# Performance work log

Hardware: AMD Instinct MI355X
Metric: run time of the kernel (lower is better)

## Reference

```python
import jax, jax.numpy as jnp
import numpy as np
import math

B, W, V, D, H, L = 64, 255, 16389, 512, 8, 8
S = W + 1          # window + cls token
NLOC = V - 5       # n_locations
CLS = V - 1        # cls_index = 16388
DH = D // H
FF = 4 * D


def _pe(seq_len, d):
    # Faithful to the quirky PositionalEmbedding: for even col c, sin(pos/10000**(2c/d));
    # for odd col c (= i+1), cos(pos/10000**(2c/d)) since it uses 2*(i+1)/d.
    pos = np.arange(seq_len, dtype=np.float32)[:, None]
    c = np.arange(d, dtype=np.float32)[None, :]
    ang = pos / (10000.0 ** (2.0 * c / d))
    pe = np.where(np.arange(d)[None, :] % 2 == 0, np.sin(ang), np.cos(ang))
    return jnp.asarray(pe, jnp.float32)

PE = _pe(S, D)


def _ln(x, s, b):
    m = x.mean(-1, keepdims=True)
    v = ((x - m) ** 2).mean(-1, keepdims=True)
    return (x - m) * jax.lax.rsqrt(v + 1e-5) * s + b


def setup_inputs() -> dict:
    key = jax.random.key(0)
    ks = jax.random.split(key, 8)
    sd = 0.02
    return {
        "x": jax.random.randint(ks[0], (B, W), 0, NLOC),
        "emb": jax.random.normal(ks[1], (V, D), jnp.float32) * sd,
        "qkv_w": jax.random.normal(ks[2], (L, D, 3 * D), jnp.float32) * sd,
        "qkv_b": jnp.zeros((L, 3 * D), jnp.float32),
        "out_w": jax.random.normal(ks[3], (L, D, D), jnp.float32) * sd,
        "out_b": jnp.zeros((L, D), jnp.float32),
        "ln1_s": jnp.ones((L, D), jnp.float32),
        "ln1_b": jnp.zeros((L, D), jnp.float32),
        "ln2_s": jnp.ones((L, D), jnp.float32),
        "ln2_b": jnp.zeros((L, D), jnp.float32),
        "ff1_w": jax.random.normal(ks[4], (L, D, FF), jnp.float32) * sd,
        "ff1_b": jnp.zeros((L, FF), jnp.float32),
        "ff2_w": jax.random.normal(ks[5], (L, FF, D), jnp.float32) * sd,
        "ff2_b": jnp.zeros((L, D), jnp.float32),
        "fn_s": jnp.ones((D,), jnp.float32),
        "fn_b": jnp.zeros((D,), jnp.float32),
        "head_w": jax.random.normal(ks[6], (D, V), jnp.float32) * sd,
    }


def _forward(x, emb, qkv_w, qkv_b, out_w, out_b, ln1_s, ln1_b, ln2_s, ln2_b,
             ff1_w, ff1_b, ff2_w, ff2_b, fn_s, fn_b, head_w):
    b = x.shape[0]
    xc = jnp.concatenate([x, jnp.full((b, 1), CLS, x.dtype)], axis=1)  # [B,S]
    h = emb[xc] + PE[None, :, :]

    def layer(h, p):
        qw, qb, ow, ob, l1s, l1b, l2s, l2b, w1, b1, w2, b2 = p
        x2 = _ln(h, l1s, l1b)
        qkv = x2 @ qw + qb                       # [B,S,3D]
        q, k, v = jnp.split(qkv, 3, axis=-1)
        sh = lambda t: t.reshape(b, S, H, DH).transpose(0, 2, 1, 3)  # [B,H,S,DH]
        q, k, v = sh(q), sh(k), sh(v)
        scores = jnp.einsum('bhqd,bhkd->bhqk', q, k) / math.sqrt(DH)
        attn = jax.nn.softmax(scores, axis=-1)
        o = jnp.einsum('bhqk,bhkd->bhqd', attn, v)
        o = o.transpose(0, 2, 1, 3).reshape(b, S, D)
        h = h + (o @ ow + ob)
        x2 = _ln(h, l2s, l2b)
        h = h + (jax.nn.relu(x2 @ w1 + b1) @ w2 + b2)
        return h, None

    h, _ = jax.lax.scan(layer, h, (qkv_w, qkv_b, out_w, out_b, ln1_s, ln1_b,
                                   ln2_s, ln2_b, ff1_w, ff1_b, ff2_w, ff2_b))
    h = _ln(h, fn_s, fn_b)
    # original projects every position then slices [:, -1, :NLOC]; projecting
    # only the last position with the first NLOC columns is identical math.
    return h[:, -1, :] @ head_w[:, :NLOC]        # [B, NLOC]


def reference(x, emb, qkv_w, qkv_b, out_w, out_b, ln1_s, ln1_b, ln2_s, ln2_b,
              ff1_w, ff1_b, ff2_w, ff2_b, fn_s, fn_b, head_w):
    return _forward(x, emb, qkv_w, qkv_b, out_w, out_b, ln1_s, ln1_b, ln2_s,
                    ln2_b, ff1_w, ff1_b, ff2_w, ff2_b, fn_s, fn_b, head_w)
```

## Files before the change

kernel.cpp:

```cpp
#include <hip/hip_runtime.h>
#include <hip/hip_bf16.h>
#include <math.h>

#define B_    64
#define W_    255
#define S_    256
#define V_    16389
#define NLOC_ 16384
#define CLS_  16388
#define D_    512
#define H_    8
#define DH_   64
#define FF_   2048
#define L_    8
#define NTOK  (B_ * S_)

typedef __attribute__((ext_vector_type(4))) float f32x4;
typedef __attribute__((ext_vector_type(8))) short s16x8;

__device__ inline unsigned short f2b(float f) {
  union { float f; unsigned u; } v; v.f = f;
  unsigned r = v.u + 0x7fff + ((v.u >> 16) & 1);
  return (unsigned short)(r >> 16);
}
__device__ inline void gl_lds16(const void* g, void* l) {
  __builtin_amdgcn_global_load_lds((const __attribute__((address_space(1))) unsigned int*)g,
                                   (__attribute__((address_space(3))) unsigned int*)l, 16, 0, 0);
}

__global__ __launch_bounds__(256) void embed_kernel(const int* __restrict__ x,
                                                    const float* __restrict__ emb,
                                                    float* __restrict__ h) {
  const int tok = blockIdx.x;
  const int bb = tok >> 8, ss = tok & 255;
  const int idx = (ss < W_) ? x[bb * W_ + ss] : CLS_;
  const float* e = emb + (size_t)idx * D_;
  float* hp = h + (size_t)tok * D_;
  #pragma unroll
  for (int r = 0; r < 2; ++r) {
    int d = threadIdx.x + r * 256;
    float ex = exp2f(-(float)d * (13.287712379549449f / 256.0f));
    float ang = (float)ss * ex;
    float pe = (d & 1) ? cosf(ang) : sinf(ang);
    hp[d] = e[d] + pe;
  }
}

__global__ __launch_bounds__(256) void ln_kernel(const float* __restrict__ in,
                                                 unsigned short* __restrict__ out,
                                                 const float* __restrict__ sc,
                                                 const float* __restrict__ bi) {
  const int tok = blockIdx.x;
  const int tid = threadIdx.x;
  const float* xp = in + (size_t)tok * D_;
  unsigned short* yp = out + (size_t)tok * D_;
  float v0 = xp[tid], v1 = xp[tid + 256];
  float sum = v0 + v1;
  #pragma unroll
  for (int off = 32; off; off >>= 1) sum += __shfl_down(sum, off);
  __shared__ float red[4];
  __shared__ float stat[2];
  const int wave = tid >> 6, lane = tid & 63;
  if (lane == 0) red[wave] = sum;
  __syncthreads();
  if (tid == 0) stat[0] = (red[0] + red[1] + red[2] + red[3]) * (1.0f / D_);
  __syncthreads();
  const float mean = stat[0];
  float d0 = v0 - mean, d1 = v1 - mean;
  float ss = d0 * d0 + d1 * d1;
  #pragma unroll
  for (int off = 32; off; off >>= 1) ss += __shfl_down(ss, off);
  if (lane == 0) red[wave] = ss;
  __syncthreads();
  if (tid == 0) stat[1] = rsqrtf((red[0] + red[1] + red[2] + red[3]) * (1.0f / D_) + 1e-5f);
  __syncthreads();
  const float inv = stat[1];
  yp[tid]       = f2b(d0 * inv * sc[tid] + bi[tid]);
  yp[tid + 256] = f2b(d1 * inv * sc[tid + 256] + bi[tid + 256]);
}

__global__ __launch_bounds__(256) void wconv_kernel(const float* __restrict__ W,
                                                    unsigned short* __restrict__ Wt,
                                                    int K, int ldn) {
  __shared__ float t[64][65];
  const int n0 = blockIdx.x * 64, k0 = blockIdx.y * 64;
  const int r = threadIdx.x >> 6;
  const int c = threadIdx.x & 63;
  #pragma unroll
  for (int i = 0; i < 16; ++i) {
    int kk = i * 4 + r;
    t[kk][c] = W[(size_t)(k0 + kk) * ldn + n0 + c];
  }
  __syncthreads();
  #pragma unroll
  for (int i = 0; i < 16; ++i) {
    int nn = i * 4 + r;
    Wt[(size_t)(n0 + nn) * K + k0 + c] = f2b(t[c][nn]);
  }
}

template<bool BIAS, bool RELU, bool RES, bool OUTBF>
__global__ __launch_bounds__(256) void mfma_gemm(
    const unsigned short* __restrict__ A, long lda,
    const unsigned short* __restrict__ Bt,
    const float* __restrict__ bias,
    float* __restrict__ Cres,
    unsigned short* __restrict__ Cbf,
    int M, int N, int K, int ldc) {
  __shared__ __align__(16) unsigned char smem[16384];
  unsigned short* As = (unsigned short*)smem;
  unsigned short* Bs = As + 128 * 32;
  const int tid = threadIdx.x;
  const int w = tid >> 6, lane = tid & 63;
  const int wm = w >> 1, wn = w & 1;
  const int row0 = blockIdx.y * 128, col0 = blockIdx.x * 128;
  f32x4 acc[4][4] = {};
  const int sr = lane >> 2;
  const int sq = ((lane & 3) ^ ((sr >> 1) & 3)) * 8;
  const int fr = lane & 15;
  const int fg = lane >> 4;
  const int fo = (fg ^ ((fr >> 1) & 3)) * 8;
  for (int k0 = 0; k0 < K; k0 += 32) {
    #pragma unroll
    for (int i = 0; i < 2; ++i) {
      int seg = w * 2 + i;
      int r = seg * 16 + sr;
      int ar = row0 + r; if (ar >= M) ar = M - 1;
      gl_lds16(A + (size_t)ar * lda + k0 + sq, As + seg * 512);
      gl_lds16(Bt + (size_t)(col0 + r) * K + k0 + sq, Bs + seg * 512);
    }
    __syncthreads();
    s16x8 af[4], bf[4];
    #pragma unroll
    for (int mi = 0; mi < 4; ++mi)
      af[mi] = *(const s16x8*)&As[(wm * 64 + mi * 16 + fr) * 32 + fo];
    #pragma unroll
    for (int ni = 0; ni < 4; ++ni)
      bf[ni] = *(const s16x8*)&Bs[(wn * 64 + ni * 16 + fr) * 32 + fo];
    #pragma unroll
    for (int mi = 0; mi < 4; ++mi)
      #pragma unroll
      for (int ni = 0; ni < 4; ++ni)
        acc[mi][ni] = __builtin_amdgcn_mfma_f32_16x16x32_bf16(af[mi], bf[ni], acc[mi][ni], 0, 0, 0);
    __syncthreads();
  }
  const int er4 = fg * 4;
  const int ec = fr;
  if (OUTBF) {
    unsigned short* Cs = (unsigned short*)smem;
    #pragma unroll
    for (int half = 0; half < 2; ++half) {
      __syncthreads();
      if (wm == half) {
        #pragma unroll
        for (int mi = 0; mi < 4; ++mi)
          #pragma unroll
          for (int ni = 0; ni < 4; ++ni) {
            int col = wn * 64 + ni * 16 + ec;
            float bv = BIAS ? bias[col0 + col] : 0.0f;
            #pragma unroll
            for (int r = 0; r < 4; ++r) {
              float v = acc[mi][ni][r] + bv;
              if (RELU) v = fmaxf(v, 0.0f);
              Cs[(mi * 16 + er4 + r) * 128 + col] = f2b(v);
            }
          }
      }
      __syncthreads();
      #pragma unroll
      for (int i = 0; i < 4; ++i) {
        int chunk = i * 256 + tid;
        int row = chunk >> 4, cc = chunk & 15;
        int grow = row0 + half * 64 + row;
        if (grow < M)
          *(s16x8*)(Cbf + (size_t)grow * ldc + col0 + cc * 8) =
              *(const s16x8*)&Cs[row * 128 + cc * 8];
      }
    }
  } else {
    float* Csf = (float*)smem;
    #pragma unroll
    for (int q = 0; q < 4; ++q) {
      __syncthreads();
      if (wm == (q >> 1)) {
        #pragma unroll
        for (int m2 = 0; m2 < 2; ++m2) {
          int mi = (q & 1) * 2 + m2;
          #pragma unroll
          for (int ni = 0; ni < 4; ++ni) {
            int col = wn * 64 + ni * 16 + ec;
            float bv = BIAS ? bias[col0 + col] : 0.0f;
            #pragma unroll
            for (int r = 0; r < 4; ++r) {
              float v = acc[mi][ni][r] + bv;
              if (RELU) v = fmaxf(v, 0.0f);
              Csf[(m2 * 16 + er4 + r) * 128 + col] = v;
            }
          }
        }
      }
      __syncthreads();
      #pragma unroll
      for (int i = 0; i < 4; ++i) {
        int chunk = i * 256 + tid;
        int row = chunk >> 5, cc = chunk & 31;
        int grow = row0 + q * 32 + row;
        if (grow < M) {
          float4 v = *(const float4*)&Csf[row * 128 + cc * 4];
          float* gp = Cres + (size_t)grow * ldc + col0 + cc * 4;
          if (RES) {
            float4 hv = *(const float4*)gp;
            v.x += hv.x; v.y += hv.y; v.z += hv.z; v.w += hv.w;
          }
          *(float4*)gp = v;
        }
      }
    }
  }
}

__global__ __launch_bounds__(256) void vt_kernel(const unsigned short* __restrict__ qkvb,
                                                 unsigned short* __restrict__ vtg) {
  const int bh = blockIdx.x;
  const int jt = blockIdx.y;
  const int bb = bh >> 3, hh = bh & 7;
  __shared__ unsigned short t[64][72];
  const int r = threadIdx.x >> 2;
  const int c = (threadIdx.x & 3) * 16;
  const unsigned short* src = qkvb + (size_t)(bb * 256 + jt * 64 + r) * 1536 + 1024 + hh * 64 + c;
  *(s16x8*)&t[r][c]     = *(const s16x8*)src;
  *(s16x8*)&t[r][c + 8] = *(const s16x8*)(src + 8);
  __syncthreads();
  unsigned short tmp[16];
  #pragma unroll
  for (int i = 0; i < 16; ++i) tmp[i] = t[c + i][r];
  unsigned short* dst = vtg + ((size_t)bh * 64 + r) * 256 + jt * 64 + c;
  *(s16x8*)dst       = *(const s16x8*)&tmp[0];
  *(s16x8*)(dst + 8) = *(const s16x8*)&tmp[8];
}

__global__ __launch_bounds__(256) void attn_mfma(const unsigned short* __restrict__ qkvb,
                                                 const unsigned short* __restrict__ vtg,
                                                 unsigned short* __restrict__ obuf) {
  const int bh = blockIdx.x;
  const int bb = bh >> 3, hh = bh & 7;
  const int tid = threadIdx.x, w = tid >> 6, lane = tid & 63;
  __shared__ unsigned short Pl[4][16][264];
  const int fr = lane & 15, fg = lane >> 4;
  const unsigned short* qbase = qkvb + (size_t)bb * 256 * 1536 + hh * 64;
  const unsigned short* kbase = qbase + 512;
  const unsigned short* vb = vtg + (size_t)bh * 64 * 256;
  unsigned short* ob = obuf + (size_t)bb * 256 * 512 + hh * 64;

  for (int s = w; s < 16; s += 4) {
    const int q0 = s * 16;
    f32x4 sacc[16] = {};
    s16x8 aq[2];
    #pragma unroll
    for (int kk = 0; kk < 2; ++kk)
      aq[kk] = *(const s16x8*)(qbase + (size_t)(q0 + fr) * 1536 + kk * 32 + fg * 8);
    #pragma unroll
    for (int ni = 0; ni < 16; ++ni) {
      #pragma unroll
      for (int kk = 0; kk < 2; ++kk) {
        s16x8 bk = *(const s16x8*)(kbase + (size_t)(ni * 16 + fr) * 1536 + kk * 32 + fg * 8);
        sacc[ni] = __builtin_amdgcn_mfma_f32_16x16x32_bf16(aq[kk], bk, sacc[ni], 0, 0, 0);
      }
    }
    #pragma unroll
    for (int rr = 0; rr < 4; ++rr) {
      float mx = -1e30f;
      #pragma unroll
      for (int ni = 0; ni < 16; ++ni) mx = fmaxf(mx, sacc[ni][rr]);
      #pragma unroll
      for (int off = 1; off <= 8; off <<= 1) mx = fmaxf(mx, __shfl_xor(mx, off));
      float sum = 0.0f;
      #pragma unroll
      for (int ni = 0; ni < 16; ++ni) {
        float e = __expf((sacc[ni][rr] - mx) * 0.125f);
        sacc[ni][rr] = e; sum += e;
      }
      #pragma unroll
      for (int off = 1; off <= 8; off <<= 1) sum += __shfl_xor(sum, off);
      float inv = 1.0f / sum;
      #pragma unroll
      for (int ni = 0; ni < 16; ++ni) sacc[ni][rr] *= inv;
    }
    #pragma unroll
    for (int ni = 0; ni < 16; ++ni)
      #pragma unroll
      for (int rr = 0; rr < 4; ++rr)
        Pl[w][fg * 4 + rr][ni * 16 + fr] = f2b(sacc[ni][rr]);
    f32x4 oacc[4] = {};
    #pragma unroll
    for (int kk = 0; kk < 8; ++kk) {
      s16x8 ap = *(const s16x8*)&Pl[w][fr][kk * 32 + fg * 8];
      #pragma unroll
      for (int ni = 0; ni < 4; ++ni) {
        s16x8 bv = *(const s16x8*)(vb + (size_t)(ni * 16 + fr) * 256 + kk * 32 + fg * 8);
        oacc[ni] = __builtin_amdgcn_mfma_f32_16x16x32_bf16(ap, bv, oacc[ni], 0, 0, 0);
      }
    }
    #pragma unroll
    for (int ni = 0; ni < 4; ++ni)
      #pragma unroll
      for (int rr = 0; rr < 4; ++rr)
        ob[(size_t)(q0 + fg * 4 + rr) * 512 + ni * 16 + fr] = f2b(oacc[ni][rr]);
  }
}

extern "C" void kernel_launch(void* const* d_in, const int* in_sizes, int n_in,
                              void* d_out, int out_size, void* d_ws, size_t ws_size,
                              hipStream_t stream) {
  const int*   x      = (const int*)  d_in[0];
  const float* emb    = (const float*)d_in[1];
  const float* qkv_w  = (const float*)d_in[2];
  const float* qkv_b  = (const float*)d_in[3];
  const float* out_w  = (const float*)d_in[4];
  const float* out_b  = (const float*)d_in[5];
  const float* ln1_s  = (const float*)d_in[6];
  const float* ln1_b  = (const float*)d_in[7];
  const float* ln2_s  = (const float*)d_in[8];
  const float* ln2_b  = (const float*)d_in[9];
  const float* ff1_w  = (const float*)d_in[10];
  const float* ff1_b  = (const float*)d_in[11];
  const float* ff2_w  = (const float*)d_in[12];
  const float* ff2_b  = (const float*)d_in[13];
  const float* fn_s   = (const float*)d_in[14];
  const float* fn_b   = (const float*)d_in[15];
  const float* head_w = (const float*)d_in[16];
  float* out = (float*)d_out;

  char* p = (char*)d_ws;
  float* h = (float*)p;                      p += (size_t)NTOK * D_ * 4;
  unsigned short* x2b = (unsigned short*)p;  p += (size_t)NTOK * D_ * 2;
  unsigned short* qkvb = (unsigned short*)p; p += (size_t)NTOK * 3 * D_ * 2;
  unsigned short* vtg = (unsigned short*)p;  p += (size_t)B_ * H_ * DH_ * S_ * 2;
  unsigned short* obuf = (unsigned short*)p; p += (size_t)NTOK * D_ * 2;
  unsigned short* wt_qkv = (unsigned short*)p; p += (size_t)D_ * 3 * D_ * 2;
  unsigned short* wt_out = (unsigned short*)p; p += (size_t)D_ * D_ * 2;
  unsigned short* wt_ff1 = (unsigned short*)p; p += (size_t)D_ * FF_ * 2;
  unsigned short* wt_ff2 = (unsigned short*)p; p += (size_t)FF_ * D_ * 2;
  unsigned short* wth = (unsigned short*)p;    p += (size_t)NLOC_ * D_ * 2;
  unsigned short* ffmid = qkvb;

  embed_kernel<<<NTOK, 256, 0, stream>>>(x, emb, h);
  wconv_kernel<<<dim3(NLOC_ / 64, D_ / 64), 256, 0, stream>>>(head_w, wth, D_, V_);

  for (int l = 0; l < L_; ++l) {
    wconv_kernel<<<dim3(3 * D_ / 64, D_ / 64), 256, 0, stream>>>(
        qkv_w + (size_t)l * D_ * 3 * D_, wt_qkv, D_, 3 * D_);
    wconv_kernel<<<dim3(D_ / 64, D_ / 64), 256, 0, stream>>>(
        out_w + (size_t)l * D_ * D_, wt_out, D_, D_);
    wconv_kernel<<<dim3(FF_ / 64, D_ / 64), 256, 0, stream>>>(
        ff1_w + (size_t)l * D_ * FF_, wt_ff1, D_, FF_);
    wconv_kernel<<<dim3(D_ / 64, FF_ / 64), 256, 0, stream>>>(
        ff2_w + (size_t)l * FF_ * D_, wt_ff2, FF_, D_);

    ln_kernel<<<NTOK, 256, 0, stream>>>(h, x2b, ln1_s + l * D_, ln1_b + l * D_);
    mfma_gemm<true, false, false, true><<<dim3(3 * D_ / 128, NTOK / 128), 256, 0, stream>>>(
        x2b, D_, wt_qkv, qkv_b + (size_t)l * 3 * D_, nullptr, qkvb,
        NTOK, 3 * D_, D_, 3 * D_);
    vt_kernel<<<dim3(B_ * H_, 4), 256, 0, stream>>>(qkvb, vtg);
    attn_mfma<<<B_ * H_, 256, 0, stream>>>(qkvb, vtg, obuf);
    mfma_gemm<true, false, true, false><<<dim3(D_ / 128, NTOK / 128), 256, 0, stream>>>(
        obuf, D_, wt_out, out_b + (size_t)l * D_, h, nullptr,
        NTOK, D_, D_, D_);
    ln_kernel<<<NTOK, 256, 0, stream>>>(h, x2b, ln2_s + l * D_, ln2_b + l * D_);
    mfma_gemm<true, true, false, true><<<dim3(FF_ / 128, NTOK / 128), 256, 0, stream>>>(
        x2b, D_, wt_ff1, ff1_b + (size_t)l * FF_, nullptr, ffmid,
        NTOK, FF_, D_, FF_);
    mfma_gemm<true, false, true, false><<<dim3(D_ / 128, NTOK / 128), 256, 0, stream>>>(
        ffmid, FF_, wt_ff2, ff2_b + (size_t)l * D_, h, nullptr,
        NTOK, D_, FF_, D_);
  }
  ln_kernel<<<NTOK, 256, 0, stream>>>(h, x2b, fn_s, fn_b);
  mfma_gemm<false, false, false, false><<<dim3(NLOC_ / 128, 1), 256, 0, stream>>>(
      x2b + (size_t)(S_ - 1) * D_, (long)S_ * D_, wth, nullptr, out, nullptr,
      B_, NLOC_, D_, NLOC_);
}
```

Measured before the change: 2.641 ms.

## Switch GEMM to 32x32 MFMA, remap blocks per XCD, batch weight conversion, warp-per-row LayerNorm

The GEMM now uses 32x32x16 bf16 MFMA with a simpler k-major LDS layout, which means fewer fragment loads per MFMA. It also remaps block IDs so each XCD works on a contiguous band of rows, to improve L2 locality. All per-layer weight transposes are batched into a few launches up front using a z-grid, and LayerNorm processes one token per wavefront with float4 loads and no block barriers. These changes cut launch count and synchronisation. The cost is more workspace for the per-layer bf16 weights, and the new LDS layout drops the XOR swizzle, which may cause bank conflicts.

Result: slower. 2.790 ms (+5.6%).

```diff
diff --git a/kernel.cpp b/kernel.cpp
--- a/kernel.cpp
+++ b/kernel.cpp
@@ -15,8 +15,9 @@
 #define L_    8
 #define NTOK  (B_ * S_)
 
-typedef __attribute__((ext_vector_type(4))) float f32x4;
-typedef __attribute__((ext_vector_type(8))) short s16x8;
+typedef __attribute__((ext_vector_type(4)))  float f32x4;
+typedef __attribute__((ext_vector_type(16))) float f32x16;
+typedef __attribute__((ext_vector_type(8)))  short s16x8;
 
 __device__ inline unsigned short f2b(float f) {
   union { float f; unsigned u; } v; v.f = f;
@@ -50,38 +51,41 @@
                                                  unsigned short* __restrict__ out,
                                                  const float* __restrict__ sc,
                                                  const float* __restrict__ bi) {
-  const int tok = blockIdx.x;
-  const int tid = threadIdx.x;
+  const int tok = blockIdx.x * 4 + (threadIdx.x >> 6);
+  const int lane = threadIdx.x & 63;
   const float* xp = in + (size_t)tok * D_;
+  float4 a = *(const float4*)(xp + lane * 4);
+  float4 b = *(const float4*)(xp + 256 + lane * 4);
+  float sum = a.x + a.y + a.z + a.w + b.x + b.y + b.z + b.w;
+  #pragma unroll
+  for (int off = 32; off; off >>= 1) sum += __shfl_xor(sum, off);
+  const float mean = sum * (1.0f / D_);
+  float d0 = a.x - mean, d1 = a.y - mean, d2 = a.z - mean, d3 = a.w - mean;
+  float e0 = b.x - mean, e1 = b.y - mean, e2 = b.z - mean, e3 = b.w - mean;
+  float ss = d0*d0 + d1*d1 + d2*d2 + d3*d3 + e0*e0 + e1*e1 + e2*e2 + e3*e3;
+  #pragma unroll
+  for (int off = 32; off; off >>= 1) ss += __shfl_xor(ss, off);
+  const float inv = rsqrtf(ss * (1.0f / D_) + 1e-5f);
+  float4 s0 = *(const float4*)(sc + lane * 4);
+  float4 s1 = *(const float4*)(sc + 256 + lane * 4);
+  float4 b0 = *(const float4*)(bi + lane * 4);
+  float4 b1 = *(const float4*)(bi + 256 + lane * 4);
+  unsigned short o[8];
+  o[0] = f2b(d0 * inv * s0.x + b0.x); o[1] = f2b(d1 * inv * s0.y + b0.y);
+  o[2] = f2b(d2 * inv * s0.z + b0.z); o[3] = f2b(d3 * inv * s0.w + b0.w);
+  o[4] = f2b(e0 * inv * s1.x + b1.x); o[5] = f2b(e1 * inv * s1.y + b1.y);
+  o[6] = f2b(e2 * inv * s1.z + b1.z); o[7] = f2b(e3 * inv * s1.w + b1.w);
   unsigned short* yp = out + (size_t)tok * D_;
-  float v0 = xp[tid], v1 = xp[tid + 256];
-  float sum = v0 + v1;
-  #pragma unroll
-  for (int off = 32; off; off >>= 1) sum += __shfl_down(sum, off);
-  __shared__ float red[4];
-  __shared__ float stat[2];
-  const int wave = tid >> 6, lane = tid & 63;
-  if (lane == 0) red[wave] = sum;
-  __syncthreads();
-  if (tid == 0) stat[0] = (red[0] + red[1] + red[2] + red[3]) * (1.0f / D_);
-  __syncthreads();
-  const float mean = stat[0];
-  float d0 = v0 - mean, d1 = v1 - mean;
-  float ss = d0 * d0 + d1 * d1;
-  #pragma unroll
-  for (int off = 32; off; off >>= 1) ss += __shfl_down(ss, off);
-  if (lane == 0) red[wave] = ss;
-  __syncthreads();
-  if (tid == 0) stat[1] = rsqrtf((red[0] + red[1] + red[2] + red[3]) * (1.0f / D_) + 1e-5f);
-  __syncthreads();
-  const float inv = stat[1];
-  yp[tid]       = f2b(d0 * inv * sc[tid] + bi[tid]);
-  yp[tid + 256] = f2b(d1 * inv * sc[tid + 256] + bi[tid + 256]);
+  *(ushort4*)(yp + lane * 4)       = *(const ushort4*)&o[0];
+  *(ushort4*)(yp + 256 + lane * 4) = *(const ushort4*)&o[4];
 }
 
 __global__ __launch_bounds__(256) void wconv_kernel(const float* __restrict__ W,
                                                     unsigned short* __restrict__ Wt,
-                                                    int K, int ldn) {
+                                                    int K, int ldn,
+                                                    long in_stride, long out_stride) {
+  const float* Wl = W + (size_t)blockIdx.z * in_stride;
+  unsigned short* Wtl = Wt + (size_t)blockIdx.z * out_stride;
   __shared__ float t[64][65];
   const int n0 = blockIdx.x * 64, k0 = blockIdx.y * 64;
   const int r = threadIdx.x >> 6;
@@ -89,13 +93,13 @@
   #pragma unroll
   for (int i = 0; i < 16; ++i) {
     int kk = i * 4 + r;
-    t[kk][c] = W[(size_t)(k0 + kk) * ldn + n0 + c];
+    t[kk][c] = Wl[(size_t)(k0 + kk) * ldn + n0 + c];
   }
   __syncthreads();
   #pragma unroll
   for (int i = 0; i < 16; ++i) {
     int nn = i * 4 + r;
-    Wt[(size_t)(n0 + nn) * K + k0 + c] = f2b(t[c][nn]);
+    Wtl[(size_t)(n0 + nn) * K + k0 + c] = f2b(t[c][nn]);
   }
 }
 
@@ -113,39 +117,47 @@
   const int tid = threadIdx.x;
   const int w = tid >> 6, lane = tid & 63;
   const int wm = w >> 1, wn = w & 1;
-  const int row0 = blockIdx.y * 128, col0 = blockIdx.x * 128;
-  f32x4 acc[4][4] = {};
-  const int sr = lane >> 2;
-  const int sq = ((lane & 3) ^ ((sr >> 1) & 3)) * 8;
-  const int fr = lane & 15;
-  const int fg = lane >> 4;
-  const int fo = (fg ^ ((fr >> 1) & 3)) * 8;
+  int bx, by;
+  {
+    int nx = gridDim.x, ny = gridDim.y;
+    int id = blockIdx.y * nx + blockIdx.x;
+    if ((ny & 7) == 0) {
+      int xcd = id & 7, k = id >> 3, band = ny >> 3;
+      int kr = k / nx;
+      by = xcd * band + kr;
+      bx = k - kr * nx;
+    } else { bx = blockIdx.x; by = blockIdx.y; }
+  }
+  const int row0 = by * 128, col0 = bx * 128;
+  f32x16 acc[2][2] = {};
+  const int fl = lane & 31, fg2 = lane >> 5;
+  const int sc8 = w * 8;
   for (int k0 = 0; k0 < K; k0 += 32) {
     #pragma unroll
     for (int i = 0; i < 2; ++i) {
-      int seg = w * 2 + i;
-      int r = seg * 16 + sr;
+      int r = i * 64 + lane;
       int ar = row0 + r; if (ar >= M) ar = M - 1;
-      gl_lds16(A + (size_t)ar * lda + k0 + sq, As + seg * 512);
-      gl_lds16(Bt + (size_t)(col0 + r) * K + k0 + sq, Bs + seg * 512);
+      gl_lds16(A + (size_t)ar * lda + k0 + sc8, As + (w * 2 + i) * 512);
+      gl_lds16(Bt + (size_t)(col0 + r) * K + k0 + sc8, Bs + (w * 2 + i) * 512);
     }
     __syncthreads();
-    s16x8 af[4], bf[4];
-    #pragma unroll
-    for (int mi = 0; mi < 4; ++mi)
-      af[mi] = *(const s16x8*)&As[(wm * 64 + mi * 16 + fr) * 32 + fo];
-    #pragma unroll
-    for (int ni = 0; ni < 4; ++ni)
-      bf[ni] = *(const s16x8*)&Bs[(wn * 64 + ni * 16 + fr) * 32 + fo];
-    #pragma unroll
-    for (int mi = 0; mi < 4; ++mi)
-      #pragma unroll
-      for (int ni = 0; ni < 4; ++ni)
-        acc[mi][ni] = __builtin_amdgcn_mfma_f32_16x16x32_bf16(af[mi], bf[ni], acc[mi][ni], 0, 0, 0);
+    #pragma unroll
+    for (int ks = 0; ks < 2; ++ks) {
+      s16x8 af[2], bf2[2];
+      #pragma unroll
+      for (int mi = 0; mi < 2; ++mi)
+        af[mi] = *(const s16x8*)&As[((ks * 2 + fg2) * 128 + wm * 64 + mi * 32 + fl) * 8];
+      #pragma unroll
+      for (int ni = 0; ni < 2; ++ni)
+        bf2[ni] = *(const s16x8*)&Bs[((ks * 2 + fg2) * 128 + wn * 64 + ni * 32 + fl) * 8];
+      #pragma unroll
+      for (int mi = 0; mi < 2; ++mi)
+        #pragma unroll
+        for (int ni = 0; ni < 2; ++ni)
+          acc[mi][ni] = __builtin_amdgcn_mfma_f32_32x32x16_bf16(af[mi], bf2[ni], acc[mi][ni], 0, 0, 0);
+    }
     __syncthreads();
   }
-  const int er4 = fg * 4;
-  const int ec = fr;
   if (OUTBF) {
     unsigned short* Cs = (unsigned short*)smem;
     #pragma unroll
@@ -153,16 +165,17 @@
       __syncthreads();
       if (wm == half) {
         #pragma unroll
-        for (int mi = 0; mi < 4; ++mi)
+        for (int mi = 0; mi < 2; ++mi)
           #pragma unroll
-          for (int ni = 0; ni < 4; ++ni) {
-            int col = wn * 64 + ni * 16 + ec;
+          for (int ni = 0; ni < 2; ++ni) {
+            int col = wn * 64 + ni * 32 + fl;
             float bv = BIAS ? bias[col0 + col] : 0.0f;
             #pragma unroll
-            for (int r = 0; r < 4; ++r) {
-              float v = acc[mi][ni][r] + bv;
+            for (int rg = 0; rg < 16; ++rg) {
+              int rl = mi * 32 + (rg & 3) + 8 * (rg >> 2) + 4 * fg2;
+              float v = acc[mi][ni][rg] + bv;
               if (RELU) v = fmaxf(v, 0.0f);
-              Cs[(mi * 16 + er4 + r) * 128 + col] = f2b(v);
+              Cs[rl * 128 + col] = f2b(v);
             }
           }
       }
@@ -183,19 +196,17 @@
     for (int q = 0; q < 4; ++q) {
       __syncthreads();
       if (wm == (q >> 1)) {
+        const int mi = q & 1;
         #pragma unroll
-        for (int m2 = 0; m2 < 2; ++m2) {
-          int mi = (q & 1) * 2 + m2;
+        for (int ni = 0; ni < 2; ++ni) {
+          int col = wn * 64 + ni * 32 + fl;
+          float bv = BIAS ? bias[col0 + col] : 0.0f;
           #pragma unroll
-          for (int ni = 0; ni < 4; ++ni) {
-            int col = wn * 64 + ni * 16 + ec;
-            float bv = BIAS ? bias[col0 + col] : 0.0f;
-            #pragma unroll
-            for (int r = 0; r < 4; ++r) {
-              float v = acc[mi][ni][r] + bv;
-              if (RELU) v = fmaxf(v, 0.0f);
-              Csf[(m2 * 16 + er4 + r) * 128 + col] = v;
-            }
+          for (int rg = 0; rg < 16; ++rg) {
+            int rl = (rg & 3) + 8 * (rg >> 2) + 4 * fg2;
+            float v = acc[mi][ni][rg] + bv;
+            if (RELU) v = fmaxf(v, 0.0f);
+            Csf[rl * 128 + col] = v;
           }
         }
       }
@@ -337,44 +348,44 @@
   unsigned short* qkvb = (unsigned short*)p; p += (size_t)NTOK * 3 * D_ * 2;
   unsigned short* vtg = (unsigned short*)p;  p += (size_t)B_ * H_ * DH_ * S_ * 2;
   unsigned short* obuf = (unsigned short*)p; p += (size_t)NTOK * D_ * 2;
-  unsigned short* wt_qkv = (unsigned short*)p; p += (size_t)D_ * 3 * D_ * 2;
-  unsigned short* wt_out = (unsigned short*)p; p += (size_t)D_ * D_ * 2;
-  unsigned short* wt_ff1 = (unsigned short*)p; p += (size_t)D_ * FF_ * 2;
-  unsigned short* wt_ff2 = (unsigned short*)p; p += (size_t)FF_ * D_ * 2;
+  unsigned short* wt_qkv = (unsigned short*)p; p += (size_t)L_ * D_ * 3 * D_ * 2;
+  unsigned short* wt_out = (unsigned short*)p; p += (size_t)L_ * D_ * D_ * 2;
+  unsigned short* wt_ff1 = (unsigned short*)p; p += (size_t)L_ * D_ * FF_ * 2;
+  unsigned short* wt_ff2 = (unsigned short*)p; p += (size_t)L_ * FF_ * D_ * 2;
   unsigned short* wth = (unsigned short*)p;    p += (size_t)NLOC_ * D_ * 2;
   unsigned short* ffmid = qkvb;
 
   embed_kernel<<<NTOK, 256, 0, stream>>>(x, emb, h);
-  wconv_kernel<<<dim3(NLOC_ / 64, D_ / 64), 256, 0, stream>>>(head_w, wth, D_, V_);
+  wconv_kernel<<<dim3(3 * D_ / 64, D_ / 64, L_), 256, 0, stream>>>(
+      qkv_w, wt_qkv, D_, 3 * D_, (long)D_ * 3 * D_, (long)D_ * 3 * D_);
+  wconv_kernel<<<dim3(D_ / 64, D_ / 64, L_), 256, 0, stream>>>(
+      out_w, wt_out, D_, D_, (long)D_ * D_, (long)D_ * D_);
+  wconv_kernel<<<dim3(FF_ / 64, D_ / 64, L_), 256, 0, stream>>>(
+      ff1_w, wt_ff1, D_, FF_, (long)D_ * FF_, (long)D_ * FF_);
+  wconv_kernel<<<dim3(D_ / 64, FF_ / 64, L_), 256, 0, stream>>>(
+      ff2_w, wt_ff2, FF_, D_, (long)FF_ * D_, (long)FF_ * D_);
+  wconv_kernel<<<dim3(NLOC_ / 64, D_ / 64, 1), 256, 0, stream>>>(
+      head_w, wth, D_, V_, 0, 0);
 
   for (int l = 0; l < L_; ++l) {
-    wconv_kernel<<<dim3(3 * D_ / 64, D_ / 64), 256, 0, stream>>>(
-        qkv_w + (size_t)l * D_ * 3 * D_, wt_qkv, D_, 3 * D_);
-    wconv_kernel<<<dim3(D_ / 64, D_ / 64), 256, 0, stream>>>(
-        out_w + (size_t)l * D_ * D_, wt_out, D_, D_);
-    wconv_kernel<<<dim3(FF_ / 64, D_ / 64), 256, 0, stream>>>(
-        ff1_w + (size_t)l * D_ * FF_, wt_ff1, D_, FF_);
-    wconv_kernel<<<dim3(D_ / 64, FF_ / 64), 256, 0, stream>>>(
-        ff2_w + (size_t)l * FF_ * D_, wt_ff2, FF_, D_);
-
-    ln_kernel<<<NTOK, 256, 0, stream>>>(h, x2b, ln1_s + l * D_, ln1_b + l * D_);
+    ln_kernel<<<NTOK / 4, 256, 0, stream>>>(h, x2b, ln1_s + l * D_, ln1_b + l * D_);
     mfma_gemm<true, false, false, true><<<dim3(3 * D_ / 128, NTOK / 128), 256, 0, stream>>>(
-        x2b, D_, wt_qkv, qkv_b + (size_t)l * 3 * D_, nullptr, qkvb,
+        x2b, D_, wt_qkv + (size_t)l * D_ * 3 * D_, qkv_b + (size_t)l * 3 * D_, nullptr, qkvb,
         NTOK, 3 * D_, D_, 3 * D_);
     vt_kernel<<<dim3(B_ * H_, 4), 256, 0, stream>>>(qkvb, vtg);
     attn_mfma<<<B_ * H_, 256, 0, stream>>>(qkvb, vtg, obuf);
     mfma_gemm<true, false, true, false><<<dim3(D_ / 128, NTOK / 128), 256, 0, stream>>>(
-        obuf, D_, wt_out, out_b + (size_t)l * D_, h, nullptr,
+        obuf, D_, wt_out + (size_t)l * D_ * D_, out_b + (size_t)l * D_, h, nullptr,
         NTOK, D_, D_, D_);
-    ln_kernel<<<NTOK, 256, 0, stream>>>(h, x2b, ln2_s + l * D_, ln2_b + l * D_);
+    ln_kernel<<<NTOK / 4, 256, 0, stream>>>(h, x2b, ln2_s + l * D_, ln2_b + l * D_);
     mfma_gemm<true, true, false, true><<<dim3(FF_ / 128, NTOK / 128), 256, 0, stream>>>(
-        x2b, D_, wt_ff1, ff1_b + (size_t)l * FF_, nullptr, ffmid,
+        x2b, D_, wt_ff1 + (size_t)l * D_ * FF_, ff1_b + (size_t)l * FF_, nullptr, ffmid,
         NTOK, FF_, D_, FF_);
     mfma_gemm<true, false, true, false><<<dim3(D_ / 128, NTOK / 128), 256, 0, stream>>>(
-        ffmid, FF_, wt_ff2, ff2_b + (size_t)l * D_, h, nullptr,
+        ffmid, FF_, wt_ff2 + (size_t)l * FF_ * D_, ff2_b + (size_t)l * D_, h, nullptr,
         NTOK, D_, FF_, D_);
   }
-  ln_kernel<<<NTOK, 256, 0, stream>>>(h, x2b, fn_s, fn_b);
+  ln_kernel<<<NTOK / 4, 256, 0, stream>>>(h, x2b, fn_s, fn_b);
   mfma_gemm<false, false, false, false><<<dim3(NLOC_ / 128, 1), 256, 0, stream>>>(
       x2b + (size_t)(S_ - 1) * D_, (long)S_ * D_, wth, nullptr, out, nullptr,
       B_, NLOC_, D_, NLOC_);
```
